# Kernel optimization log

Hardware: AMD Instinct MI355X
Metric: run time of the kernel (lower is better)

## Reference

```python
import jax, jax.numpy as jnp
import numpy as np

K = 3  # involution kernel size
G = 8  # groups


def setup_inputs() -> dict:
    key = jax.random.key(0)
    ks = jax.random.split(key, 5)
    b, c, h, w = 8, 64, 128, 128
    r = 2
    x = jax.random.normal(ks[0], (b, c, h, w), dtype=jnp.float32)
    w_reduce = jax.random.normal(ks[1], (c // r, c), dtype=jnp.float32) * 0.1
    b_reduce = jax.random.normal(ks[2], (c // r,), dtype=jnp.float32) * 0.1
    w_span = jax.random.normal(ks[3], (K * K * G, c // r), dtype=jnp.float32) * 0.1
    b_span = jax.random.normal(ks[4], (K * K * G,), dtype=jnp.float32) * 0.1
    return {"x": x, "w_reduce": w_reduce, "b_reduce": b_reduce,
            "w_span": w_span, "b_span": b_span}


def reference(x, w_reduce, b_reduce, w_span, b_span):
    b, c, h, w = x.shape
    # kernel generation: two 1x1 convs (ss=1 so AvgPool is identity)
    y = jnp.einsum('oc,bchw->bohw', w_reduce, x) + b_reduce[None, :, None, None]
    kern = jnp.einsum('oc,bchw->bohw', w_span, y) + b_span[None, :, None, None]
    kern = kern.reshape(b, G, K * K, h, w)  # per-pixel dynamic kernel
    # unfold: k=3, padding=1, stride=1 -> patches ordered (c, kh, kw) like nn.Unfold
    xp = jnp.pad(x, ((0, 0), (0, 0), (1, 1), (1, 1)))
    patches = jnp.stack([xp[:, :, i:i + h, j:j + w]
                         for i in range(K) for j in range(K)], axis=2)  # (b,c,9,h,w)
    patches = patches.reshape(b, G, c // G, K * K, h, w)
    # multiply by dynamic kernel (broadcast over c//G) and reduce over k*k
    out = jnp.einsum('bgkhw,bgckhw->bgchw', kern, patches)
    return out.reshape(b, c, h, w)
```

## Files before the change

### kernel.cpp

```cpp
#include <hip/hip_runtime.h>


#define HW 16384
#define WPX 128

__global__ void invol_setup(const float* __restrict__ w_reduce,
                            const float* __restrict__ b_reduce,
                            const float* __restrict__ w_span,
                            const float* __restrict__ b_span,
                            float* __restrict__ ws)
{
    const int tid = blockIdx.x * 256 + threadIdx.x;
    if (tid >= 72 * 64) return;
    const int row = tid >> 6;
    const int c   = tid & 63;
    float s = 0.f;
#pragma unroll
    for (int i = 0; i < 32; ++i)
        s = fmaf(w_span[row * 32 + i], w_reduce[i * 64 + c], s);
    ws[72 + (row / 9) * 576 + c * 9 + (row % 9)] = s;
    if (c == 0) {
        float t = b_span[row];
#pragma unroll
        for (int i = 0; i < 32; ++i)
            t = fmaf(w_span[row * 32 + i], b_reduce[i], t);
        ws[row] = t;
    }
}

#define PHA_LD(XV, C0)                                                        \
    _Pragma("unroll")                                                         \
    for (int i = 0; i < 16; ++i)                                              \
        XV[i] = *reinterpret_cast<const float2*>(xb + (size_t)((C0) + i) * HW);

#define PHA_FMA(XV, C0)                                                       \
    _Pragma("unroll")                                                         \
    for (int i = 0; i < 16; ++i) {                                            \
        _Pragma("unroll")                                                     \
        for (int j = 0; j < 9; ++j) {                                         \
            const float wv = Wg[((C0) + i) * 9 + j];                          \
            kg[j].x = fmaf(wv, XV[i].x, kg[j].x);                             \
            kg[j].y = fmaf(wv, XV[i].y, kg[j].y);                             \
        }                                                                     \
    }

__global__ __launch_bounds__(256, 4) void invol_main(
    const float* __restrict__ x,
    const float* __restrict__ ws,
    float* __restrict__ out)
{
    const int bid     = blockIdx.x;
    const int logical = (bid & 7) * 256 + (bid >> 3);
    const int o  = logical & 7;
    const int pb = logical >> 3;

    const int P2  = pb * 256 + threadIdx.x;
    const int b   = P2 >> 13;
    const int hw0 = (P2 & 8191) << 1;
    const int h   = hw0 >> 7;
    const int w0  = hw0 & 127;

    const size_t imgoff = (size_t)b * 64 * HW;
    const float* xb  = x + imgoff + hw0;
    const float* Wg  = ws + 72 + o * 576;
    const float* bbg = ws + o * 9;

    float2 kg[9];
#pragma unroll
    for (int j = 0; j < 9; ++j) { const float t = bbg[j]; kg[j] = make_float2(t, t); }

    {
        float2 xv0[16], xv1[16];
        PHA_LD(xv0, 0)
        PHA_LD(xv1, 16)
        PHA_FMA(xv0, 0)
        PHA_LD(xv0, 32)
        PHA_FMA(xv1, 16)
        PHA_LD(xv1, 48)
        PHA_FMA(xv0, 32)
        PHA_FMA(xv1, 48)
    }

    int rof[3];
#pragma unroll
    for (int t = 0; t < 3; ++t) {
        const int hh = h + t - 1;
        const int hc = hh < 0 ? 0 : (hh > 127 ? 127 : hh);
        rof[t] = (hc - h) * WPX;
        const float m = ((unsigned)hh < 128u) ? 1.f : 0.f;
#pragma unroll
        for (int d = 0; d < 3; ++d) { kg[t * 3 + d].x *= m; kg[t * 3 + d].y *= m; }
    }
    const int dwl = (w0 == 0)   ? 0 : -1;
    const int dwr = (w0 == 126) ? 1 : 2;
    if (w0 == 0)   { kg[0].x = 0.f; kg[3].x = 0.f; kg[6].x = 0.f; }
    if (w0 == 126) { kg[2].y = 0.f; kg[5].y = 0.f; kg[8].y = 0.f; }

    float2 vC[24];
    float  vL[24], vR[24];
#pragma unroll
    for (int ci = 0; ci < 8; ++ci) {
        const float* xc = xb + (size_t)(o * 8 + ci) * HW;
#pragma unroll
        for (int t = 0; t < 3; ++t) {
            vC[ci * 3 + t] = *reinterpret_cast<const float2*>(xc + rof[t]);
            vL[ci * 3 + t] = xc[rof[t] + dwl];
            vR[ci * 3 + t] = xc[rof[t] + dwr];
        }
    }
#pragma unroll
    for (int ci = 0; ci < 8; ++ci) {
        float acc0 = 0.f, acc1 = 0.f;
#pragma unroll
        for (int t = 0; t < 3; ++t) {
            acc0 = fmaf(kg[t * 3 + 0].x, vL[ci * 3 + t],   acc0);
            acc0 = fmaf(kg[t * 3 + 1].x, vC[ci * 3 + t].x, acc0);
            acc0 = fmaf(kg[t * 3 + 2].x, vC[ci * 3 + t].y, acc0);
            acc1 = fmaf(kg[t * 3 + 0].y, vC[ci * 3 + t].x, acc1);
            acc1 = fmaf(kg[t * 3 + 1].y, vC[ci * 3 + t].y, acc1);
            acc1 = fmaf(kg[t * 3 + 2].y, vR[ci * 3 + t],   acc1);
        }
        *reinterpret_cast<float2*>(out + imgoff + (size_t)(o * 8 + ci) * HW + hw0) =
            make_float2(acc0, acc1);
    }
}

__global__ __launch_bounds__(256) void invol_fused_fallback(
    const float* __restrict__ x,
    const float* __restrict__ w_reduce,
    const float* __restrict__ b_reduce,
    const float* __restrict__ w_span,
    const float* __restrict__ b_span,
    float* __restrict__ out)
{
    const int pid = blockIdx.x * 256 + threadIdx.x;
    const int b  = pid >> 14;
    const int hw = pid & 16383;
    const int h  = hw >> 7;
    const int w  = hw & 127;
    const float* xb   = x   + (size_t)b * 64 * HW + hw;
    float*       outb = out + (size_t)b * 64 * HW + hw;
    float y[32];
#pragma unroll
    for (int o = 0; o < 32; ++o) y[o] = b_reduce[o];
#pragma unroll 4
    for (int c = 0; c < 64; ++c) {
        const float xc = xb[(size_t)c * HW];
#pragma unroll
        for (int o = 0; o < 32; ++o)
            y[o] = fmaf(w_reduce[o * 64 + c], xc, y[o]);
    }
    for (int g = 0; g < 8; ++g) {
        float kg[9];
#pragma unroll
        for (int k = 0; k < 9; ++k) {
            float s = b_span[g * 9 + k];
#pragma unroll
            for (int i = 0; i < 32; ++i)
                s = fmaf(w_span[(g * 9 + k) * 32 + i], y[i], s);
            kg[k] = s;
        }
#pragma unroll
        for (int ci = 0; ci < 8; ++ci) {
            const int c = g * 8 + ci;
            const float* xc = xb + (size_t)c * HW;
            float acc = 0.f;
#pragma unroll
            for (int k = 0; k < 9; ++k) {
                const int dh = k / 3 - 1, dw = k % 3 - 1;
                const int hh = h + dh, ww = w + dw;
                float v = ((unsigned)hh < 128u && (unsigned)ww < 128u)
                          ? xc[dh * WPX + dw] : 0.f;
                acc = fmaf(kg[k], v, acc);
            }
            outb[(size_t)c * HW] = acc;
        }
    }
}

extern "C" void kernel_launch(void* const* d_in, const int* in_sizes, int n_in,
                              void* d_out, int out_size, void* d_ws, size_t ws_size,
                              hipStream_t stream) {
    const float* x        = (const float*)d_in[0];
    const float* w_reduce = (const float*)d_in[1];
    const float* b_reduce = (const float*)d_in[2];
    const float* w_span   = (const float*)d_in[3];
    const float* b_span   = (const float*)d_in[4];
    float* out = (float*)d_out;

    const size_t ws_needed = (size_t)(72 + 8 * 64 * 9) * sizeof(float);
    if (ws_size >= ws_needed) {
        float* ws = (float*)d_ws;
        invol_setup<<<18, 256, 0, stream>>>(w_reduce, b_reduce, w_span, b_span, ws);
        const int npairs = 8 * 128 * 128 / 2;
        invol_main<<<npairs / 256 * 8, 256, 0, stream>>>(x, ws, out);
    } else {
        const int npix = 8 * 128 * 128;
        invol_fused_fallback<<<npix / 256, 256, 0, stream>>>(
            x, w_reduce, b_reduce, w_span, b_span, out);
    }
}
```

Before: 51.19 us.

## Software-pipeline channel loads across kernel-generation and involution phases

Splits the 64-channel kernel-generation pass into 8-channel chunks with a triple-buffered register rotation, and issues the neighborhood loads for the involution phase early, interleaved with the last generation FMAs. Scheduling barriers keep the compiler from reordering the loads and compute, so global memory latency overlaps arithmetic across both phases. Row masking is deferred until generation finishes. This raises register pressure under the 4-waves-per-SIMD launch bound and risks spills.

```diff
diff --git a/kernel.cpp b/kernel.cpp
--- a/kernel.cpp
+++ b/kernel.cpp
@@ -3,6 +3,7 @@
 
 #define HW 16384
 #define WPX 128
+#define SB() __builtin_amdgcn_sched_barrier(0)
 
 __global__ void invol_setup(const float* __restrict__ w_reduce,
                             const float* __restrict__ b_reduce,
@@ -28,20 +29,47 @@
     }
 }
 
-#define PHA_LD(XV, C0)                                                        \
+#define LDA(BUF, C0)                                                          \
     _Pragma("unroll")                                                         \
-    for (int i = 0; i < 16; ++i)                                              \
-        XV[i] = *reinterpret_cast<const float2*>(xb + (size_t)((C0) + i) * HW);
-
-#define PHA_FMA(XV, C0)                                                       \
+    for (int i = 0; i < 8; ++i)                                               \
+        BUF[i] = *reinterpret_cast<const float2*>(xb + (size_t)((C0) + i) * HW);
+
+#define FMAA(BUF, C0)                                                         \
     _Pragma("unroll")                                                         \
-    for (int i = 0; i < 16; ++i) {                                            \
+    for (int i = 0; i < 8; ++i) {                                             \
         _Pragma("unroll")                                                     \
         for (int j = 0; j < 9; ++j) {                                         \
             const float wv = Wg[((C0) + i) * 9 + j];                          \
-            kg[j].x = fmaf(wv, XV[i].x, kg[j].x);                             \
-            kg[j].y = fmaf(wv, XV[i].y, kg[j].y);                             \
+            kg[j].x = fmaf(wv, BUF[i].x, kg[j].x);                            \
+            kg[j].y = fmaf(wv, BUF[i].y, kg[j].y);                            \
         }                                                                     \
+    }
+
+#define LDB(CI)                                                               \
+    {                                                                         \
+        const float* xc = xb + (size_t)(o * 8 + (CI)) * HW;                   \
+        _Pragma("unroll")                                                     \
+        for (int t = 0; t < 3; ++t) {                                         \
+            vC[(CI) * 3 + t] = *reinterpret_cast<const float2*>(xc + rof[t]); \
+            vL[(CI) * 3 + t] = xc[rof[t] + dwl];                              \
+            vR[(CI) * 3 + t] = xc[rof[t] + dwr];                              \
+        }                                                                     \
+    }
+
+#define FMAB(CI)                                                              \
+    {                                                                         \
+        float acc0 = 0.f, acc1 = 0.f;                                         \
+        _Pragma("unroll")                                                     \
+        for (int t = 0; t < 3; ++t) {                                         \
+            acc0 = fmaf(kg[t * 3 + 0].x, vL[(CI) * 3 + t],   acc0);           \
+            acc0 = fmaf(kg[t * 3 + 1].x, vC[(CI) * 3 + t].x, acc0);           \
+            acc0 = fmaf(kg[t * 3 + 2].x, vC[(CI) * 3 + t].y, acc0);           \
+            acc1 = fmaf(kg[t * 3 + 0].y, vC[(CI) * 3 + t].x, acc1);           \
+            acc1 = fmaf(kg[t * 3 + 1].y, vC[(CI) * 3 + t].y, acc1);           \
+            acc1 = fmaf(kg[t * 3 + 2].y, vR[(CI) * 3 + t],   acc1);           \
+        }                                                                     \
+        *reinterpret_cast<float2*>(out + imgoff + (size_t)(o * 8 + (CI)) * HW \
+                                   + hw0) = make_float2(acc0, acc1);          \
     }
 
 __global__ __launch_bounds__(256, 4) void invol_main(
@@ -65,64 +93,68 @@
     const float* Wg  = ws + 72 + o * 576;
     const float* bbg = ws + o * 9;
 
-    float2 kg[9];
-#pragma unroll
-    for (int j = 0; j < 9; ++j) { const float t = bbg[j]; kg[j] = make_float2(t, t); }
-
-    {
-        float2 xv0[16], xv1[16];
-        PHA_LD(xv0, 0)
-        PHA_LD(xv1, 16)
-        PHA_FMA(xv0, 0)
-        PHA_LD(xv0, 32)
-        PHA_FMA(xv1, 16)
-        PHA_LD(xv1, 48)
-        PHA_FMA(xv0, 32)
-        PHA_FMA(xv1, 48)
-    }
-
-    int rof[3];
+    int   rof[3];
+    float rmask[3];
 #pragma unroll
     for (int t = 0; t < 3; ++t) {
         const int hh = h + t - 1;
         const int hc = hh < 0 ? 0 : (hh > 127 ? 127 : hh);
-        rof[t] = (hc - h) * WPX;
-        const float m = ((unsigned)hh < 128u) ? 1.f : 0.f;
-#pragma unroll
-        for (int d = 0; d < 3; ++d) { kg[t * 3 + d].x *= m; kg[t * 3 + d].y *= m; }
+        rof[t]   = (hc - h) * WPX;
+        rmask[t] = ((unsigned)hh < 128u) ? 1.f : 0.f;
     }
     const int dwl = (w0 == 0)   ? 0 : -1;
     const int dwr = (w0 == 126) ? 1 : 2;
+
+    float2 kg[9];
+#pragma unroll
+    for (int j = 0; j < 9; ++j) { const float t = bbg[j]; kg[j] = make_float2(t, t); }
+
+    float2 xva[8], xvb[8], xvc[8];
+    float2 vC[24];
+    float  vL[24], vR[24];
+
+    LDA(xva, 0)
+    LDA(xvb, 8)
+    LDA(xvc, 16)
+    SB();
+    FMAA(xva, 0)  LDA(xva, 24)
+    SB();
+    FMAA(xvb, 8)  LDA(xvb, 32)
+    SB();
+    FMAA(xvc, 16) LDA(xvc, 40)
+    SB();
+    FMAA(xva, 24) LDA(xva, 48)
+    SB();
+    FMAA(xvb, 32) LDA(xvb, 56)
+    SB();
+    FMAA(xvc, 40) LDB(0) LDB(1)
+    SB();
+    FMAA(xva, 48) LDB(2) LDB(3)
+    SB();
+    FMAA(xvb, 56) LDB(4) LDB(5)
+    SB();
+
+#pragma unroll
+    for (int t = 0; t < 3; ++t) {
+#pragma unroll
+        for (int d = 0; d < 3; ++d) {
+            kg[t * 3 + d].x *= rmask[t];
+            kg[t * 3 + d].y *= rmask[t];
+        }
+    }
     if (w0 == 0)   { kg[0].x = 0.f; kg[3].x = 0.f; kg[6].x = 0.f; }
     if (w0 == 126) { kg[2].y = 0.f; kg[5].y = 0.f; kg[8].y = 0.f; }
 
-    float2 vC[24];
-    float  vL[24], vR[24];
-#pragma unroll
-    for (int ci = 0; ci < 8; ++ci) {
-        const float* xc = xb + (size_t)(o * 8 + ci) * HW;
-#pragma unroll
-        for (int t = 0; t < 3; ++t) {
-            vC[ci * 3 + t] = *reinterpret_cast<const float2*>(xc + rof[t]);
-            vL[ci * 3 + t] = xc[rof[t] + dwl];
-            vR[ci * 3 + t] = xc[rof[t] + dwr];
-        }
-    }
-#pragma unroll
-    for (int ci = 0; ci < 8; ++ci) {
-        float acc0 = 0.f, acc1 = 0.f;
-#pragma unroll
-        for (int t = 0; t < 3; ++t) {
-            acc0 = fmaf(kg[t * 3 + 0].x, vL[ci * 3 + t],   acc0);
-            acc0 = fmaf(kg[t * 3 + 1].x, vC[ci * 3 + t].x, acc0);
-            acc0 = fmaf(kg[t * 3 + 2].x, vC[ci * 3 + t].y, acc0);
-            acc1 = fmaf(kg[t * 3 + 0].y, vC[ci * 3 + t].x, acc1);
-            acc1 = fmaf(kg[t * 3 + 1].y, vC[ci * 3 + t].y, acc1);
-            acc1 = fmaf(kg[t * 3 + 2].y, vR[ci * 3 + t],   acc1);
-        }
-        *reinterpret_cast<float2*>(out + imgoff + (size_t)(o * 8 + ci) * HW + hw0) =
-            make_float2(acc0, acc1);
-    }
+    FMAB(0)
+    FMAB(1)
+    LDB(6) LDB(7)
+    SB();
+    FMAB(2)
+    FMAB(3)
+    FMAB(4)
+    FMAB(5)
+    FMAB(6)
+    FMAB(7)
 }
 
 __global__ __launch_bounds__(256) void invol_fused_fallback(
```

After: 133.7 us. +161.1%, slower.
